# Kernel optimization log

Measured on AMD Instinct MI355X. Metric: run time of the kernel, lower is better.

## Reference

```python
import jax, jax.numpy as jnp
import numpy as np
import math

VOCAB = 32000
D = 128           # embedding_size
S = 4096          # max_seq_len
B = 4
N_W = math.ceil(math.log2(S))   # 12
K = N_W + 1                      # n_links = 13


def _chord_cols():
    # col[i, 0] = i ; col[i, k] = (i + 2**(k-1)) % S  for k = 1..K-1
    i = np.arange(S)[:, None]
    offs = np.concatenate([[0], 2 ** np.arange(K - 1)])
    return jnp.asarray((i + offs[None, :]) % S, dtype=jnp.int32)


def setup_inputs() -> dict:
    key = jax.random.key(0)
    ks = jax.random.split(key, 8)
    sc = 0.02
    return {
        "data": jax.random.randint(ks[0], (B, S), 0, VOCAB),
        "cols": _chord_cols(),
        "emb": jax.random.normal(ks[1], (VOCAB, D), jnp.float32) * sc,
        "apc": jax.random.normal(ks[2], (S, D), jnp.float32) * sc,
        "g_W1": jax.random.normal(ks[3], (D, D), jnp.float32) * sc,
        "g_b1": jnp.zeros((D,), jnp.float32),
        "g_W2": jax.random.normal(ks[4], (D, D), jnp.float32) * sc,
        "g_b2": jnp.zeros((D,), jnp.float32),
        "f_W1": jax.random.normal(ks[5], (N_W, D, D), jnp.float32) * sc,
        "f_b1": jnp.zeros((N_W, D), jnp.float32),
        "f_W2": jax.random.normal(ks[6], (N_W, D, K), jnp.float32) * sc,
        "f_b2": jnp.zeros((N_W, K), jnp.float32),
    }


def reference(data, cols, emb, apc, g_W1, g_b1, g_W2, g_b2, f_W1, f_b1, f_W2, f_b2):
    # token + absolute position embeddings (dropouts are identity in eval)
    x = emb[data] + apc[None, :, :]                       # [B, S, D]
    # V = g(x): Linear -> GELU -> Linear
    V = jax.nn.gelu(x @ g_W1 + g_b1, approximate=False) @ g_W2 + g_b2  # [B, S, D]
    res = V
    # Precompute all n_W per-position mixing weight tensors W_m = f_m(x)
    h = jax.nn.gelu(jnp.einsum('bsd,mde->mbse', x, f_W1) + f_b1[:, None, None, :],
                    approximate=False)                    # [M, B, S, D]
    W_all = jnp.einsum('mbse,mek->mbsk', h, f_W2) + f_b2[:, None, None, :]  # [M, B, S, K]

    def step(V, W_m):
        # chord spmm: out[b,i,:] = sum_k W_m[b,i,k] * V[b, cols[i,k], :]
        V = jnp.einsum('bsk,bskd->bsd', W_m, V[:, cols, :]) + res
        return V, None

    V, _ = jax.lax.scan(step, V, W_all)
    return V
```

## Files before the change

kernel.cpp:

```cpp
#include <hip/hip_runtime.h>
#include <hip/hip_bf16.h>

typedef __bf16 bf16x8 __attribute__((ext_vector_type(8)));
typedef float  f32x4  __attribute__((ext_vector_type(4)));
typedef unsigned short u16x8 __attribute__((ext_vector_type(8)));

#define NTOK 16384
#define SEQ  4096
#define DIM  128
#define NSEG 13
#define NM   12
#define NK   13

__device__ inline unsigned short f2bf(float f) {
    unsigned int u = __float_as_uint(f);
    unsigned int r = (u + 0x7FFFu + ((u >> 16) & 1u)) >> 16;
    return (unsigned short)r;
}
__device__ inline float bf2f(unsigned short h) {
    return __uint_as_float(((unsigned int)h) << 16);
}
__device__ inline unsigned int cvtpk(float a, float b) {
    unsigned int r;
    asm("v_cvt_pk_bf16_f32 %0, %1, %2" : "=v"(r) : "v"(a), "v"(b));
    return r;
}

__device__ inline float gelu_f(float u) {
    const float c0 = 0.3989422804f;
    const float c1 = -0.0664903801f;
    const float c2 = 0.0099735570f;
    float u2 = u * u;
    float p  = __builtin_fmaf(u2, c2, c1);
    p        = __builtin_fmaf(u2, p, c0);
    return __builtin_fmaf(u2, p, 0.5f * u);
}

__device__ inline int swz(int u16idx) {
    int byte = u16idx << 1;
    byte ^= ((byte >> 8) & 7) << 4;
    return byte >> 1;
}

#define EMB_BLOCKS 8192
#define CONV_BLOCKS ((NSEG * DIM * DIM + 255) / 256)
__global__ __launch_bounds__(256) void prep_kernel(
    const int* __restrict__ data, const float* __restrict__ emb,
    const float* __restrict__ apc, unsigned short* __restrict__ xb,
    const float* __restrict__ g_W1, const float* __restrict__ g_W2,
    const float* __restrict__ f_W1, const float* __restrict__ f_W2,
    unsigned short* __restrict__ wb1T, unsigned short* __restrict__ wb2Tg,
    unsigned short* __restrict__ wb2Tf)
{
    int tid = threadIdx.x;
    if (blockIdx.x < EMB_BLOCKS) {
        int n = blockIdx.x * 2 + (tid >> 7);
        int d = tid & 127;
        int s = n & (SEQ - 1);
        int tok = data[n];
        float v = emb[(size_t)tok * DIM + d] + apc[s * DIM + d];
        xb[(size_t)n * DIM + d] = f2bf(v);
    } else {
        int i = (blockIdx.x - EMB_BLOCKS) * 256 + tid;
        if (i < NSEG * DIM * DIM) {
            int seg = i >> 14;
            int e = (i >> 7) & 127;
            int d = i & 127;
            float v = (seg == 0) ? g_W1[d * DIM + e]
                                 : f_W1[((seg - 1) * DIM + d) * DIM + e];
            wb1T[i] = f2bf(v);
        }
        if (i < DIM * DIM) {
            int c = i >> 7, e = i & 127;
            wb2Tg[i] = f2bf(g_W2[e * DIM + c]);
        }
        if (i < NM * 16 * DIM) {
            int m = i >> 11;
            int c = (i >> 7) & 15;
            int e = i & 127;
            float v = (c < NK) ? f_W2[(m * DIM + e) * NK + c] : 0.f;
            wb2Tf[i] = f2bf(v);
        }
    }
}

__global__ __launch_bounds__(256, 3) void mlp_kernel(
    const unsigned short* __restrict__ xb,
    const unsigned short* __restrict__ wb1T,
    const unsigned short* __restrict__ wb2Tg,
    const unsigned short* __restrict__ wb2Tf,
    const float* __restrict__ g_b1, const float* __restrict__ g_b2,
    const float* __restrict__ f_b1, const float* __restrict__ f_b2,
    float* __restrict__ resF, unsigned short* __restrict__ resB,
    unsigned short* __restrict__ Wallb)
{
    const int seg  = blockIdx.y;
    const int row0 = blockIdx.x * 64;
    const int tid  = threadIdx.x;
    const int wave = tid >> 6;
    const int lane = tid & 63;

    __shared__ __align__(16) unsigned short Hs[4][16 * DIM];
    __shared__ __align__(16) unsigned short W1s[DIM * DIM];
    __shared__ __align__(16) unsigned short W2fs[16 * DIM];

    const int r16   = lane & 15;
    const int kgrp  = (lane >> 4) * 8;
    const int crow0 = (lane >> 4) << 2;

    const float* b1p = (seg == 0) ? g_b1 : (f_b1 + (seg - 1) * DIM);
    float bias1[8];
    #pragma unroll
    for (int t = 0; t < 8; ++t) bias1[t] = b1p[t * 16 + r16];
    float bias2[8];
    float bias2f = 0.f;
    if (seg == 0) {
        #pragma unroll
        for (int t = 0; t < 8; ++t) bias2[t] = g_b2[t * 16 + r16];
    } else {
        bias2f = (r16 < NK) ? f_b2[(seg - 1) * NK + r16] : 0.f;
    }

    {
        const int4* wg = reinterpret_cast<const int4*>(wb1T + (size_t)seg * DIM * DIM);
        #pragma unroll
        for (int i = 0; i < 8; ++i)
            *reinterpret_cast<int4*>(&W1s[swz((tid + i * 256) * 8)]) = wg[tid + i * 256];
    }
    if (seg != 0) {
        const int4* wg = reinterpret_cast<const int4*>(wb2Tf + (size_t)(seg - 1) * 16 * DIM);
        *reinterpret_cast<int4*>(&W2fs[swz(tid * 8)]) = wg[tid];
    }
    __syncthreads();

    const unsigned short* xrow = xb + (size_t)(row0 + wave * 16 + r16) * DIM + kgrp;
    f32x4 acc[8];
    #pragma unroll
    for (int t = 0; t < 8; ++t) acc[t] = (f32x4){0.f, 0.f, 0.f, 0.f};
    #pragma unroll
    for (int kk = 0; kk < 4; ++kk) {
        bf16x8 a = *reinterpret_cast<const bf16x8*>(xrow + kk * 32);
        #pragma unroll
        for (int t = 0; t < 8; ++t) {
            bf16x8 b = *reinterpret_cast<const bf16x8*>(&W1s[swz((t * 16 + r16) * DIM + kk * 32 + kgrp)]);
            acc[t] = __builtin_amdgcn_mfma_f32_16x16x32_bf16(a, b, acc[t], 0, 0, 0);
        }
    }

    unsigned short* hs = Hs[wave];
    #pragma unroll
    for (int t = 0; t < 8; ++t) {
        int col = t * 16 + r16;
        #pragma unroll
        for (int r = 0; r < 4; r += 2) {
            float g0 = gelu_f(acc[t][r]     + bias1[t]);
            float g1 = gelu_f(acc[t][r + 1] + bias1[t]);
            unsigned int pk = cvtpk(g0, g1);
            hs[swz((crow0 + r)     * DIM + col)] = (unsigned short)pk;
            hs[swz((crow0 + r + 1) * DIM + col)] = (unsigned short)(pk >> 16);
        }
    }

    if (seg == 0) {
        f32x4 acc2[8];
        #pragma unroll
        for (int t = 0; t < 8; ++t) acc2[t] = (f32x4){0.f, 0.f, 0.f, 0.f};
        #pragma unroll
        for (int kk = 0; kk < 4; ++kk) {
            bf16x8 a = *reinterpret_cast<const bf16x8*>(&hs[swz(r16 * DIM + kk * 32 + kgrp)]);
            #pragma unroll
            for (int t = 0; t < 8; ++t) {
                bf16x8 b = *reinterpret_cast<const bf16x8*>(wb2Tg + (size_t)(t * 16 + r16) * DIM + kk * 32 + kgrp);
                acc2[t] = __builtin_amdgcn_mfma_f32_16x16x32_bf16(a, b, acc2[t], 0, 0, 0);
            }
        }
        #pragma unroll
        for (int t = 0; t < 8; ++t) {
            int col = t * 16 + r16;
            #pragma unroll
            for (int r = 0; r < 4; r += 2) {
                int grow = row0 + wave * 16 + crow0 + r;
                float v0 = acc2[t][r]     + bias2[t];
                float v1 = acc2[t][r + 1] + bias2[t];
                resF[(size_t)grow * DIM + col]       = v0;
                resF[(size_t)(grow + 1) * DIM + col] = v1;
                unsigned int pk = cvtpk(v0, v1);
                resB[(size_t)grow * DIM + col]       = (unsigned short)pk;
                resB[(size_t)(grow + 1) * DIM + col] = (unsigned short)(pk >> 16);
            }
        }
    } else {
        int m = seg - 1;
        f32x4 acc2 = (f32x4){0.f, 0.f, 0.f, 0.f};
        #pragma unroll
        for (int kk = 0; kk < 4; ++kk) {
            bf16x8 a = *reinterpret_cast<const bf16x8*>(&hs[swz(r16 * DIM + kk * 32 + kgrp)]);
            bf16x8 b = *reinterpret_cast<const bf16x8*>(&W2fs[swz(r16 * DIM + kk * 32 + kgrp)]);
            acc2 = __builtin_amdgcn_mfma_f32_16x16x32_bf16(a, b, acc2, 0, 0, 0);
        }
        #pragma unroll
        for (int r = 0; r < 4; r += 2) {
            int grow = row0 + wave * 16 + crow0 + r;
            unsigned int pk = cvtpk(acc2[r] + bias2f, acc2[r + 1] + bias2f);
            Wallb[((size_t)m * NTOK + grow) * 16 + r16]     = (unsigned short)pk;
            Wallb[((size_t)m * NTOK + grow + 1) * 16 + r16] = (unsigned short)(pk >> 16);
        }
    }
}

#define CCH 2
#define PADTOK (SEQ + 2048)
__global__ __launch_bounds__(1024) void scan_lds_kernel(
    const unsigned short* __restrict__ resB,
    const float* __restrict__ resF,
    const unsigned short* __restrict__ Wallb,
    float* __restrict__ outF)
{
    __shared__ unsigned int V32[2 * PADTOK];

    const int bb  = blockIdx.x >> 6;
    const int d0  = (blockIdx.x & 63) * CCH;
    const int tid = threadIdx.x;

    float resLo[4], resHi[4];
    #pragma unroll
    for (int j = 0; j < 4; ++j) {
        int t = j * 1024 + tid;
        int n = (bb << 12) + t;
        unsigned int r = *reinterpret_cast<const unsigned int*>(resB + (size_t)n * DIM + d0);
        resLo[j] = __uint_as_float(r << 16);
        resHi[j] = __uint_as_float(r & 0xffff0000u);
        V32[t] = r;
        if (j < 2) V32[t + SEQ] = r;
    }
    __syncthreads();

    const unsigned short* wb0 = Wallb + (size_t)(bb << 12) * 16;
    unsigned int curbase = 0;

    #pragma unroll 1
    for (int m = 0; m < NM - 1; ++m) {
        const unsigned short* wp = wb0 + (size_t)m * NTOK * 16;
        const unsigned int nb = curbase ^ PADTOK;
        float oL[4], oH[4];
        #pragma unroll
        for (int j = 0; j < 4; ++j) {
            const int t = j * 1024 + tid;
            const uint4* wrow = reinterpret_cast<const uint4*>(wp + (size_t)t * 16);
            uint4 wa = wrow[0];
            uint4 wb = wrow[1];
            float o0 = resLo[j], o1 = resHi[j];
            const unsigned int* vb = &V32[curbase + t];
            #pragma unroll
            for (int k = 0; k < NK; ++k) {
                const int off = (k == 0) ? 0 : (1 << (k - 1));
                unsigned int ww =
                    (k < 2) ? wa.x : (k < 4) ? wa.y : (k < 6) ? wa.z : (k < 8) ? wa.w :
                    (k < 10) ? wb.x : (k < 12) ? wb.y : wb.z;
                float w = (k & 1) ? __uint_as_float(ww & 0xffff0000u)
                                  : __uint_as_float(ww << 16);
                unsigned int v = vb[off];
                o0 = __builtin_fmaf(w, __uint_as_float(v << 16),          o0);
                o1 = __builtin_fmaf(w, __uint_as_float(v & 0xffff0000u), o1);
            }
            oL[j] = o0; oH[j] = o1;
        }
        #pragma unroll
        for (int j = 0; j < 4; ++j) {
            int t = j * 1024 + tid;
            unsigned int pk = cvtpk(oL[j], oH[j]);
            V32[nb + t] = pk;
            if (j < 2) V32[nb + t + SEQ] = pk;
        }
        __syncthreads();
        curbase = nb;
    }

    {
        const unsigned short* wp = wb0 + (size_t)(NM - 1) * NTOK * 16;
        #pragma unroll
        for (int j = 0; j < 4; ++j) {
            const int t = j * 1024 + tid;
            const int n = (bb << 12) + t;
            const uint4* wrow = reinterpret_cast<const uint4*>(wp + (size_t)t * 16);
            uint4 wa = wrow[0];
            uint4 wb = wrow[1];
            float2 rf = *reinterpret_cast<const float2*>(resF + (size_t)n * DIM + d0);
            float o0 = rf.x, o1 = rf.y;
            const unsigned int* vb = &V32[curbase + t];
            #pragma unroll
            for (int k = 0; k < NK; ++k) {
                const int off = (k == 0) ? 0 : (1 << (k - 1));
                unsigned int ww =
                    (k < 2) ? wa.x : (k < 4) ? wa.y : (k < 6) ? wa.z : (k < 8) ? wa.w :
                    (k < 10) ? wb.x : (k < 12) ? wb.y : wb.z;
                float w = (k & 1) ? __uint_as_float(ww & 0xffff0000u)
                                  : __uint_as_float(ww << 16);
                unsigned int v = vb[off];
                o0 = __builtin_fmaf(w, __uint_as_float(v << 16),          o0);
                o1 = __builtin_fmaf(w, __uint_as_float(v & 0xffff0000u), o1);
            }
            float2 o; o.x = o0; o.y = o1;
            *reinterpret_cast<float2*>(outF + (size_t)n * DIM + d0) = o;
        }
    }
}

extern "C" void kernel_launch(void* const* d_in, const int* in_sizes, int n_in,
                              void* d_out, int out_size, void* d_ws, size_t ws_size,
                              hipStream_t stream) {
    const int*   data = (const int*)  d_in[0];
    const float* emb  = (const float*)d_in[2];
    const float* apc  = (const float*)d_in[3];
    const float* g_W1 = (const float*)d_in[4];
    const float* g_b1 = (const float*)d_in[5];
    const float* g_W2 = (const float*)d_in[6];
    const float* g_b2 = (const float*)d_in[7];
    const float* f_W1 = (const float*)d_in[8];
    const float* f_b1 = (const float*)d_in[9];
    const float* f_W2 = (const float*)d_in[10];
    const float* f_b2 = (const float*)d_in[11];
    float* out = (float*)d_out;

    char* ws = (char*)d_ws;
    size_t off = 0;
    auto alloc = [&](size_t bytes) {
        void* p = ws + off;
        off += (bytes + 255) & ~(size_t)255;
        return p;
    };
    unsigned short* xb    = (unsigned short*)alloc((size_t)NTOK * DIM * 2);
    unsigned short* wb1T  = (unsigned short*)alloc((size_t)NSEG * DIM * DIM * 2);
    unsigned short* wb2Tg = (unsigned short*)alloc((size_t)DIM * DIM * 2);
    unsigned short* wb2Tf = (unsigned short*)alloc((size_t)NM * 16 * DIM * 2);
    float*          resF  = (float*)alloc((size_t)NTOK * DIM * 4);
    unsigned short* resB  = (unsigned short*)alloc((size_t)NTOK * DIM * 2);
    unsigned short* Wallb = (unsigned short*)alloc((size_t)NM * NTOK * 16 * 2);
    (void)ws_size; (void)in_sizes; (void)n_in; (void)out_size;

    prep_kernel<<<EMB_BLOCKS + CONV_BLOCKS, 256, 0, stream>>>(
        data, emb, apc, xb, g_W1, g_W2, f_W1, f_W2, wb1T, wb2Tg, wb2Tf);

    dim3 grid(NTOK / 64, NSEG);
    mlp_kernel<<<grid, 256, 0, stream>>>(xb, wb1T, wb2Tg, wb2Tf,
                                         g_b1, g_b2, f_b1, f_b2, resF, resB, Wallb);

    scan_lds_kernel<<<256, 1024, 0, stream>>>(resB, resF, Wallb, out);
}
```

Measured before the change: 86.93 us.

## Assign adjacent token pairs per thread in chord scan with vector LDS reads

Each thread in the LDS scan kernel now owns two adjacent token pairs, t2/t2+1 and t2+2048/t2+2049, instead of four tokens strided by 1024. The pairing lets it read neighbours as 64-bit LDS loads and reuse its own previous outputs kept in registers for the offset-0 and offset-1 terms. It also shrinks the wraparound pad to 512 entries, handling the 2048 offset through a precomputed index. Block indices are remapped so neighbouring blocks go to different batches and chunks. This cuts LDS load instruction count and shared-memory footprint, at the cost of more live registers.

```diff
diff --git a/kernel.cpp b/kernel.cpp
--- a/kernel.cpp
+++ b/kernel.cpp
@@ -20,6 +20,7 @@
 __device__ inline float bf2f(unsigned short h) {
     return __uint_as_float(((unsigned int)h) << 16);
 }
+__device__ inline float uaf(unsigned int u) { return __uint_as_float(u); }
 __device__ inline unsigned int cvtpk(float a, float b) {
     unsigned int r;
     asm("v_cvt_pk_bf16_f32 %0, %1, %2" : "=v"(r) : "v"(a), "v"(b));
@@ -209,100 +210,166 @@
 }
 
 #define CCH 2
-#define PADTOK (SEQ + 2048)
+#define RPAD 512
+#define WTOT (SEQ + RPAD)
 __global__ __launch_bounds__(1024) void scan_lds_kernel(
     const unsigned short* __restrict__ resB,
     const float* __restrict__ resF,
     const unsigned short* __restrict__ Wallb,
     float* __restrict__ outF)
 {
-    __shared__ unsigned int V32[2 * PADTOK];
-
-    const int bb  = blockIdx.x >> 6;
-    const int d0  = (blockIdx.x & 63) * CCH;
+    __shared__ __align__(16) unsigned int V32[2 * WTOT];
+
+    const int bid = (int)blockIdx.x;
+    const int bb    = (bid >> 1) & 3;
+    const int chunk = ((bid >> 3) << 1) | (bid & 1);
+    const int d0  = chunk * CCH;
     const int tid = threadIdx.x;
-
-    float resLo[4], resHi[4];
-    #pragma unroll
-    for (int j = 0; j < 4; ++j) {
-        int t = j * 1024 + tid;
-        int n = (bb << 12) + t;
-        unsigned int r = *reinterpret_cast<const unsigned int*>(resB + (size_t)n * DIM + d0);
-        resLo[j] = __uint_as_float(r << 16);
-        resHi[j] = __uint_as_float(r & 0xffff0000u);
-        V32[t] = r;
-        if (j < 2) V32[t + SEQ] = r;
-    }
+    const int t2  = tid * 2;
+    const int b10off = (t2 < 1024) ? (3072 + t2) : (t2 - 1024);
+
+    uint2 resA, resBw, BvA, BvB;
+    {
+        const size_t nA0 = (size_t)((bb << 12) + t2);
+        unsigned int a0 = *reinterpret_cast<const unsigned int*>(resB + nA0 * DIM + d0);
+        unsigned int a1 = *reinterpret_cast<const unsigned int*>(resB + (nA0 + 1) * DIM + d0);
+        unsigned int b0 = *reinterpret_cast<const unsigned int*>(resB + (nA0 + 2048) * DIM + d0);
+        unsigned int b1 = *reinterpret_cast<const unsigned int*>(resB + (nA0 + 2049) * DIM + d0);
+        resA = make_uint2(a0, a1);
+        resBw = make_uint2(b0, b1);
+        BvA = resA; BvB = resBw;
+        *reinterpret_cast<uint2*>(&V32[t2]) = resA;
+        *reinterpret_cast<uint2*>(&V32[2048 + t2]) = resBw;
+        if (t2 < RPAD) *reinterpret_cast<uint2*>(&V32[SEQ + t2]) = resA;
+    }
+    const unsigned short* wb0 = Wallb + (size_t)(bb << 12) * 16;
     __syncthreads();
 
-    const unsigned short* wb0 = Wallb + (size_t)(bb << 12) * 16;
-    unsigned int curbase = 0;
+    unsigned int cur = 0;
 
     #pragma unroll 1
     for (int m = 0; m < NM - 1; ++m) {
         const unsigned short* wp = wb0 + (size_t)m * NTOK * 16;
-        const unsigned int nb = curbase ^ PADTOK;
+
+        unsigned int w[4][7];
+        #pragma unroll
+        for (int jj = 0; jj < 4; ++jj) {
+            const int row = (jj < 2) ? (t2 + jj) : (2048 + t2 + (jj - 2));
+            const unsigned int* wr = reinterpret_cast<const unsigned int*>(wp + (size_t)row * 16);
+            uint4 a = *reinterpret_cast<const uint4*>(wr);
+            uint2 b = *reinterpret_cast<const uint2*>(wr + 4);
+            w[jj][0] = a.x; w[jj][1] = a.y; w[jj][2] = a.z; w[jj][3] = a.w;
+            w[jj][4] = b.x; w[jj][5] = b.y; w[jj][6] = wr[6];
+        }
+
+        uint2 pA[9], pB[9];
+        #pragma unroll
+        for (int q = 1; q <= 9; ++q) {
+            pA[q - 1] = *reinterpret_cast<const uint2*>(&V32[cur + t2 + (1 << q)]);
+            pB[q - 1] = *reinterpret_cast<const uint2*>(&V32[cur + 2048 + t2 + (1 << q)]);
+        }
+        uint2 pA10 = *reinterpret_cast<const uint2*>(&V32[cur + t2 + 1024]);
+        uint2 pB10 = *reinterpret_cast<const uint2*>(&V32[cur + b10off]);
+        __builtin_amdgcn_sched_barrier(0);
+
         float oL[4], oH[4];
-        #pragma unroll
-        for (int j = 0; j < 4; ++j) {
-            const int t = j * 1024 + tid;
-            const uint4* wrow = reinterpret_cast<const uint4*>(wp + (size_t)t * 16);
-            uint4 wa = wrow[0];
-            uint4 wb = wrow[1];
-            float o0 = resLo[j], o1 = resHi[j];
-            const unsigned int* vb = &V32[curbase + t];
+        oL[0] = uaf(resA.x << 16);  oH[0] = uaf(resA.x & 0xffff0000u);
+        oL[1] = uaf(resA.y << 16);  oH[1] = uaf(resA.y & 0xffff0000u);
+        oL[2] = uaf(resBw.x << 16); oH[2] = uaf(resBw.x & 0xffff0000u);
+        oL[3] = uaf(resBw.y << 16); oH[3] = uaf(resBw.y & 0xffff0000u);
+
+        #pragma unroll
+        for (int k = 0; k < NK; ++k) {
+            unsigned int v0, v1, v2, v3;
+            if (k == 0)       { v0 = BvA.x;        v1 = BvA.y;        v2 = BvB.x;        v3 = BvB.y; }
+            else if (k == 1)  { v0 = BvA.y;        v1 = pA[0].x;      v2 = BvB.y;        v3 = pB[0].x; }
+            else if (k <= 10) { v0 = pA[k - 2].x;  v1 = pA[k - 2].y;  v2 = pB[k - 2].x;  v3 = pB[k - 2].y; }
+            else if (k == 11) { v0 = pA10.x;       v1 = pA10.y;       v2 = pB10.x;       v3 = pB10.y; }
+            else              { v0 = BvB.x;        v1 = BvB.y;        v2 = BvA.x;        v3 = BvA.y; }
             #pragma unroll
-            for (int k = 0; k < NK; ++k) {
-                const int off = (k == 0) ? 0 : (1 << (k - 1));
-                unsigned int ww =
-                    (k < 2) ? wa.x : (k < 4) ? wa.y : (k < 6) ? wa.z : (k < 8) ? wa.w :
-                    (k < 10) ? wb.x : (k < 12) ? wb.y : wb.z;
-                float w = (k & 1) ? __uint_as_float(ww & 0xffff0000u)
-                                  : __uint_as_float(ww << 16);
-                unsigned int v = vb[off];
-                o0 = __builtin_fmaf(w, __uint_as_float(v << 16),          o0);
-                o1 = __builtin_fmaf(w, __uint_as_float(v & 0xffff0000u), o1);
+            for (int jj = 0; jj < 4; ++jj) {
+                unsigned int ww = w[jj][k >> 1];
+                float wv = (k & 1) ? uaf(ww & 0xffff0000u) : uaf(ww << 16);
+                unsigned int v = (jj == 0) ? v0 : (jj == 1) ? v1 : (jj == 2) ? v2 : v3;
+                oL[jj] = __builtin_fmaf(wv, uaf(v << 16),          oL[jj]);
+                oH[jj] = __builtin_fmaf(wv, uaf(v & 0xffff0000u), oH[jj]);
             }
-            oL[j] = o0; oH[j] = o1;
-        }
-        #pragma unroll
-        for (int j = 0; j < 4; ++j) {
-            int t = j * 1024 + tid;
-            unsigned int pk = cvtpk(oL[j], oH[j]);
-            V32[nb + t] = pk;
-            if (j < 2) V32[nb + t + SEQ] = pk;
-        }
+        }
+
+        const unsigned int nb = cur ^ WTOT;
+        uint2 wa, wbv;
+        wa.x  = cvtpk(oL[0], oH[0]);  wa.y  = cvtpk(oL[1], oH[1]);
+        wbv.x = cvtpk(oL[2], oH[2]);  wbv.y = cvtpk(oL[3], oH[3]);
+        BvA = wa; BvB = wbv;
+        *reinterpret_cast<uint2*>(&V32[nb + t2]) = wa;
+        *reinterpret_cast<uint2*>(&V32[nb + 2048 + t2]) = wbv;
+        if (t2 < RPAD) *reinterpret_cast<uint2*>(&V32[nb + SEQ + t2]) = wa;
         __syncthreads();
-        curbase = nb;
+        cur = nb;
     }
 
     {
         const unsigned short* wp = wb0 + (size_t)(NM - 1) * NTOK * 16;
-        #pragma unroll
-        for (int j = 0; j < 4; ++j) {
-            const int t = j * 1024 + tid;
-            const int n = (bb << 12) + t;
-            const uint4* wrow = reinterpret_cast<const uint4*>(wp + (size_t)t * 16);
-            uint4 wa = wrow[0];
-            uint4 wb = wrow[1];
-            float2 rf = *reinterpret_cast<const float2*>(resF + (size_t)n * DIM + d0);
-            float o0 = rf.x, o1 = rf.y;
-            const unsigned int* vb = &V32[curbase + t];
+        const size_t nA0 = (size_t)((bb << 12) + t2);
+
+        float2 rf[4];
+        rf[0] = *reinterpret_cast<const float2*>(resF + nA0 * DIM + d0);
+        rf[1] = *reinterpret_cast<const float2*>(resF + (nA0 + 1) * DIM + d0);
+        rf[2] = *reinterpret_cast<const float2*>(resF + (nA0 + 2048) * DIM + d0);
+        rf[3] = *reinterpret_cast<const float2*>(resF + (nA0 + 2049) * DIM + d0);
+
+        unsigned int w[4][7];
+        #pragma unroll
+        for (int jj = 0; jj < 4; ++jj) {
+            const int row = (jj < 2) ? (t2 + jj) : (2048 + t2 + (jj - 2));
+            const unsigned int* wr = reinterpret_cast<const unsigned int*>(wp + (size_t)row * 16);
+            uint4 a = *reinterpret_cast<const uint4*>(wr);
+            uint2 b = *reinterpret_cast<const uint2*>(wr + 4);
+            w[jj][0] = a.x; w[jj][1] = a.y; w[jj][2] = a.z; w[jj][3] = a.w;
+            w[jj][4] = b.x; w[jj][5] = b.y; w[jj][6] = wr[6];
+        }
+
+        uint2 pA[9], pB[9];
+        #pragma unroll
+        for (int q = 1; q <= 9; ++q) {
+            pA[q - 1] = *reinterpret_cast<const uint2*>(&V32[cur + t2 + (1 << q)]);
+            pB[q - 1] = *reinterpret_cast<const uint2*>(&V32[cur + 2048 + t2 + (1 << q)]);
+        }
+        uint2 pA10 = *reinterpret_cast<const uint2*>(&V32[cur + t2 + 1024]);
+        uint2 pB10 = *reinterpret_cast<const uint2*>(&V32[cur + b10off]);
+        __builtin_amdgcn_sched_barrier(0);
+
+        float oL[4], oH[4];
+        #pragma unroll
+        for (int jj = 0; jj < 4; ++jj) { oL[jj] = rf[jj].x; oH[jj] = rf[jj].y; }
+
+        #pragma unroll
+        for (int k = 0; k < NK; ++k) {
+            unsigned int v0, v1, v2, v3;
+            if (k == 0)       { v0 = BvA.x;        v1 = BvA.y;        v2 = BvB.x;        v3 = BvB.y; }
+            else if (k == 1)  { v0 = BvA.y;        v1 = pA[0].x;      v2 = BvB.y;        v3 = pB[0].x; }
+            else if (k <= 10) { v0 = pA[k - 2].x;  v1 = pA[k - 2].y;  v2 = pB[k - 2].x;  v3 = pB[k - 2].y; }
+            else if (k == 11) { v0 = pA10.x;       v1 = pA10.y;       v2 = pB10.x;       v3 = pB10.y; }
+            else              { v0 = BvB.x;        v1 = BvB.y;        v2 = BvA.x;        v3 = BvA.y; }
             #pragma unroll
-            for (int k = 0; k < NK; ++k) {
-                const int off = (k == 0) ? 0 : (1 << (k - 1));
-                unsigned int ww =
-                    (k < 2) ? wa.x : (k < 4) ? wa.y : (k < 6) ? wa.z : (k < 8) ? wa.w :
-                    (k < 10) ? wb.x : (k < 12) ? wb.y : wb.z;
-                float w = (k & 1) ? __uint_as_float(ww & 0xffff0000u)
-                                  : __uint_as_float(ww << 16);
-                unsigned int v = vb[off];
-                o0 = __builtin_fmaf(w, __uint_as_float(v << 16),          o0);
-                o1 = __builtin_fmaf(w, __uint_as_float(v & 0xffff0000u), o1);
+            for (int jj = 0; jj < 4; ++jj) {
+                unsigned int ww = w[jj][k >> 1];
+                float wv = (k & 1) ? uaf(ww & 0xffff0000u) : uaf(ww << 16);
+                unsigned int v = (jj == 0) ? v0 : (jj == 1) ? v1 : (jj == 2) ? v2 : v3;
+                oL[jj] = __builtin_fmaf(wv, uaf(v << 16),          oL[jj]);
+                oH[jj] = __builtin_fmaf(wv, uaf(v & 0xffff0000u), oH[jj]);
             }
-            float2 o; o.x = o0; o.y = o1;
-            *reinterpret_cast<float2*>(outF + (size_t)n * DIM + d0) = o;
-        }
+        }
+
+        float2 o;
+        o.x = oL[0]; o.y = oH[0];
+        *reinterpret_cast<float2*>(outF + nA0 * DIM + d0) = o;
+        o.x = oL[1]; o.y = oH[1];
+        *reinterpret_cast<float2*>(outF + (nA0 + 1) * DIM + d0) = o;
+        o.x = oL[2]; o.y = oH[2];
+        *reinterpret_cast<float2*>(outF + (nA0 + 2048) * DIM + d0) = o;
+        o.x = oL[3]; o.y = oH[3];
+        *reinterpret_cast<float2*>(outF + (nA0 + 2049) * DIM + d0) = o;
     }
 }
 
```

Measured after the change: 81.95 us. 1.06x faster.
